# Kernel optimization log

Measured on AMD Instinct MI355X. Metric: run time of the kernel, lower is better.

Reference implementation:

```python
import jax, jax.numpy as jnp
import numpy as np

N_POINTS = 1_000_000
NUM_PILLARS = 30_000
BN_EPS = 1e-3


def _bn(x, gamma, beta, mean, var):
    # eval-mode BatchNorm1d with eps=0.001
    return (x - mean) * (gamma * jax.lax.rsqrt(var + BN_EPS)) + beta


def setup_inputs() -> dict:
    key = jax.random.key(0)
    ks = jax.random.split(key, 5)
    C1, C2 = 32, 64
    return {
        "points": jax.random.normal(ks[0], (N_POINTS, 5), dtype=jnp.float32),
        "f_center": jax.random.normal(ks[1], (N_POINTS, 3), dtype=jnp.float32),
        "unq_inv": jax.random.randint(ks[2], (N_POINTS,), 0, NUM_PILLARS, dtype=jnp.int32),
        "W1": jax.random.normal(ks[3], (7, C1), dtype=jnp.float32) * 0.1,
        "g1": jnp.ones((C1,), jnp.float32),
        "b1": jnp.zeros((C1,), jnp.float32),
        "m1": jnp.zeros((C1,), jnp.float32),
        "v1": jnp.ones((C1,), jnp.float32),
        "W2": jax.random.normal(ks[4], (C2, C1), dtype=jnp.float32) * 0.1,
        "g2": jnp.ones((C1,), jnp.float32),
        "b2": jnp.zeros((C1,), jnp.float32),
        "m2": jnp.zeros((C1,), jnp.float32),
        "v2": jnp.ones((C1,), jnp.float32),
    }


def reference(points, f_center, unq_inv, W1, g1, b1, m1, v1, W2, g2, b2, m2, v2):
    # gen_feat: concat(f_center, points[:,1:]) -> Linear(no bias) -> BN -> ReLU
    feats = jnp.concatenate([f_center, points[:, 1:]], axis=-1)  # [N, 7]
    h = jnp.maximum(_bn(feats @ W1, g1, b1, m1, v1), 0.0)        # [N, 32]

    # scatter_mean over pillars, then gather back and concat
    seg_sum = jax.ops.segment_sum(h, unq_inv, num_segments=NUM_PILLARS)
    counts = jax.ops.segment_sum(jnp.ones((h.shape[0],), h.dtype), unq_inv,
                                 num_segments=NUM_PILLARS)
    seg_mean = seg_sum / jnp.maximum(counts, 1.0)[:, None]       # [P, 32]
    h2 = jnp.concatenate([h, seg_mean[unq_inv]], axis=1)         # [N, 64]

    # AVFEO: Linear(64,32,no bias) -> BN -> ReLU
    out_fc = jnp.maximum(_bn(h2 @ W2, g2, b2, m2, v2), 0.0)      # [N, 32]

    # scatter_max over pillars (empty pillars -> 0, as torch_scatter)
    seg_max = jax.ops.segment_max(out_fc, unq_inv, num_segments=NUM_PILLARS)
    return jnp.where(jnp.isfinite(seg_max), seg_max, 0.0)        # [P, 32]
```

## Files before the change

### kernel.cpp

```cpp
#include <hip/hip_runtime.h>

typedef __attribute__((ext_vector_type(8))) short short8;
typedef __attribute__((ext_vector_type(4))) float floatx4;

static constexpr float EPS = 1e-3f;

#define CAP8  88
#define NB1   64
#define CCAP  20480
#define FCAP  384

#define P_W1F  0
#define P_B1F  224
#define P_W2L  256
#define P_B2F  1280
#define P_W2UT 1312
#define PREP_F 2048

__device__ __forceinline__ unsigned short f2bf(float x) {
  unsigned u = __float_as_uint(x);
  u += 0x7FFFu + ((u >> 16) & 1u);
  return (unsigned short)(u >> 16);
}

__global__ __launch_bounds__(256)
void k_prep_row8(const float* __restrict__ points, const float* __restrict__ fc,
                 int* __restrict__ tails, float* __restrict__ row8,
                 const float* __restrict__ W1, const float* __restrict__ g1,
                 const float* __restrict__ b1, const float* __restrict__ m1,
                 const float* __restrict__ v1,
                 const float* __restrict__ W2, const float* __restrict__ g2,
                 const float* __restrict__ b2, const float* __restrict__ m2,
                 const float* __restrict__ v2, float* __restrict__ prep,
                 int N) {
  const int gid = blockIdx.x * 256 + threadIdx.x;
  if (gid < 4096) tails[gid] = 0;
  if (blockIdx.x == 0) {
    const int t = threadIdx.x;
    for (int i = t; i < 224; i += 256) {
      int c = i & 31;
      prep[P_W1F + i] = W1[i] * (g1[c] * rsqrtf(v1[c] + EPS));
    }
    if (t < 32) {
      float s1 = g1[t] * rsqrtf(v1[t] + EPS);
      float s2 = g2[t] * rsqrtf(v2[t] + EPS);
      prep[P_B1F + t] = b1[t] - m1[t] * s1;
      prep[P_B2F + t] = b2[t] - m2[t] * s2;
    }
    unsigned short* wt = (unsigned short*)(prep + P_W2UT);
    for (int i = t; i < 1024; i += 256) {
      int k = i >> 5, c = i & 31;
      float s2 = g2[c] * rsqrtf(v2[c] + EPS);
      prep[P_W2L + i] = W2[(32 + k) * 32 + c] * s2;
      wt[c * 32 + k] = f2bf(W2[k * 32 + c] * s2);
    }
  }
  if (gid < N) {
    const size_t i = (size_t)gid;
    float4 a, b;
    a.x = fc[3 * i];     a.y = fc[3 * i + 1]; a.z = fc[3 * i + 2];
    a.w = points[5 * i + 1];
    b.x = points[5 * i + 2]; b.y = points[5 * i + 3]; b.z = points[5 * i + 4];
    b.w = 0.f;
    float4* dst = (float4*)(row8 + i * 8);
    dst[0] = a;
    dst[1] = b;
  }
}

__global__ __launch_bounds__(256)
void k_bin1(const int* __restrict__ unq, int* __restrict__ tails,
            int2* __restrict__ cbuf, int N) {
  __shared__ int2 orec[2048];
  __shared__ int dst[2048];
  __shared__ int hist[NB1], sbase[NB1], gbase[NB1];

  const int t = threadIdx.x;
  const int tile0 = blockIdx.x * 2048;
  const int ntile = min(2048, N - tile0);
  if (t < NB1) hist[t] = 0;
  __syncthreads();

  int pv[8], rr[8], bb[8];
  const int lbase = t * 8;
  if (lbase < ntile) {
    const int4* u4 = (const int4*)(unq + tile0 + lbase);
    int4 ua = u4[0], ub = u4[1];
    pv[0] = ua.x; pv[1] = ua.y; pv[2] = ua.z; pv[3] = ua.w;
    pv[4] = ub.x; pv[5] = ub.y; pv[6] = ub.z; pv[7] = ub.w;
#pragma unroll
    for (int u = 0; u < 8; ++u) {
      bb[u] = pv[u] >> 9;
      rr[u] = atomicAdd(&hist[bb[u]], 1);
    }
  } else {
#pragma unroll
    for (int u = 0; u < 8; ++u) bb[u] = -1;
  }
  __syncthreads();

  if (t < 64) {
    const int h = hist[t];
    int x = h;
    for (int d = 1; d < 64; d <<= 1) {
      int y = __shfl_up(x, d);
      if (t >= d) x += y;
    }
    sbase[t] = x - h;
    gbase[t] = (h > 0) ? atomicAdd(&tails[t], h) : 0;
  }
  __syncthreads();

  if (bb[0] >= 0) {
#pragma unroll
    for (int u = 0; u < 8; ++u) {
      const int s = sbase[bb[u]] + rr[u];
      orec[s] = make_int2(tile0 + lbase + u, pv[u]);
      const int gd = gbase[bb[u]] + rr[u];
      dst[s] = (gd < CCAP) ? (bb[u] * CCAP + gd) : -1;
    }
  }
  __syncthreads();

  for (int k = t; k < ntile; k += 256) {
    const int d = dst[k];
    if (d >= 0) cbuf[d] = orec[k];
  }
}

__global__ __launch_bounds__(256)
void k_bin2(const int* __restrict__ tails_ro, int* __restrict__ tails,
            const int2* __restrict__ cbuf, int2* __restrict__ fgbuf) {
  __shared__ int2 orec[2048];
  __shared__ int dst[2048];
  __shared__ int hist[64], sbase[64], gbase[64];

  const int b = blockIdx.x / 10, tl = blockIdx.x % 10;
  const int n_b = min(tails_ro[b], CCAP);
  const int tile0 = tl * 2048;
  const int ntile = min(2048, n_b - tile0);
  if (ntile <= 0) return;

  const int t = threadIdx.x;
  if (t < 64) hist[t] = 0;
  __syncthreads();

  const int2* src = cbuf + (size_t)b * CCAP + tile0;
  int2 rv[8];
  int rr[8], bb[8];
  const int lbase = t * 8;
#pragma unroll
  for (int u = 0; u < 8; ++u) {
    const int j = lbase + u;
    if (j < ntile) {
      rv[u] = src[j];
      bb[u] = (rv[u].y >> 3) & 63;
      rr[u] = atomicAdd(&hist[bb[u]], 1);
    } else bb[u] = -1;
  }
  __syncthreads();

  if (t < 64) {
    const int h = hist[t];
    int x = h;
    for (int d = 1; d < 64; d <<= 1) {
      int y = __shfl_up(x, d);
      if (t >= d) x += y;
    }
    sbase[t] = x - h;
    gbase[t] = (h > 0) ? atomicAdd(&tails[64 + (b << 6) + t], h) : 0;
  }
  __syncthreads();

#pragma unroll
  for (int u = 0; u < 8; ++u) {
    if (bb[u] >= 0) {
      const int s = sbase[bb[u]] + rr[u];
      orec[s] = rv[u];
      const int gd = gbase[bb[u]] + rr[u];
      dst[s] = (gd < FCAP) ? (((b << 6) + bb[u]) * FCAP + gd) : -1;
    }
  }
  __syncthreads();

  for (int k = t; k < ntile; k += 256) {
    const int d = dst[k];
    if (d >= 0) fgbuf[d] = orec[k];
  }
}

__global__ __launch_bounds__(512)
void k_pillar(const float* __restrict__ prep, const int* __restrict__ tails,
              const int2* __restrict__ fgbuf, const float* __restrict__ row8,
              float* __restrict__ out, int npil) {
  __shared__ __align__(16) float rec[FCAP][8];
  __shared__ unsigned short ord[8][CAP8];
  __shared__ __align__(16) unsigned short hbuf[8 * CAP8 * 32];
  __shared__ __align__(16) unsigned short w2t[1024];
  __shared__ __align__(16) float sumb[8][32];
  __shared__ int cnt8[8];

  const int t = threadIdx.x;
  if (t < 256) ((uint2*)w2t)[t] = ((const uint2*)(prep + P_W2UT))[t];
  if (t < 8) cnt8[t] = 0;
  __syncthreads();

  const int fb = blockIdx.x;
  const int nrec = min(tails[64 + fb], FCAP);

  const int2* src = fgbuf + (size_t)fb * FCAP;
  for (int j = t; j < nrec; j += 512) {
    const int2 r = src[j];
    const floatx4* rp = (const floatx4*)(row8 + (size_t)r.x * 8);
    ((floatx4*)rec[j])[0] = rp[0];
    ((floatx4*)rec[j])[1] = rp[1];
    const int pl = r.y & 7;
    const int slot = atomicAdd(&cnt8[pl], 1);
    if (slot < CAP8) ord[pl][slot] = (unsigned short)j;
  }
  __syncthreads();

  const int w = t >> 6, lane = t & 63;
  const int c = lane & 31, half = lane >> 5;
  const int p = fb * 8 + w;
  if (p >= npil) return;
  int n = cnt8[w];
  n = n < CAP8 ? n : CAP8;

  float w1c[7];
#pragma unroll
  for (int r = 0; r < 7; ++r) w1c[r] = prep[P_W1F + r * 32 + c];
  const float b1c = prep[P_B1F + c];
  const float b2c = prep[P_B2F + c];

  float ps = 0.f;
  const int rbase = w * CAP8;
#pragma unroll 2
  for (int s = half; s < n; s += 2) {
    const int j = ord[w][s];
    const floatx4 fa = *(const floatx4*)rec[j];
    const floatx4 fv = *(const floatx4*)(rec[j] + 4);
    float d = fa.x * w1c[0];
    d = fmaf(fa.y, w1c[1], d);
    d = fmaf(fa.z, w1c[2], d);
    d = fmaf(fa.w, w1c[3], d);
    d = fmaf(fv.x, w1c[4], d);
    d = fmaf(fv.y, w1c[5], d);
    d = fmaf(fv.z, w1c[6], d);
    const float h = fmaxf(d + b1c, 0.f);
    ps += h;
    const int row = rbase + s;
    hbuf[row * 32 + (c ^ (((row >> 1) & 3) << 3))] = f2bf(h);
  }
  ps += __shfl_xor(ps, 32);
  if (half == 0) sumb[w][c] = ps;
  __builtin_amdgcn_wave_barrier();

  float acc = 0.f;
  const floatx4* sb4 = (const floatx4*)sumb[w];
#pragma unroll
  for (int kq = 0; kq < 8; ++kq) {
    floatx4 sv = sb4[kq];
    acc = fmaf(sv.x, prep[P_W2L + (kq * 4 + 0) * 32 + c], acc);
    acc = fmaf(sv.y, prep[P_W2L + (kq * 4 + 1) * 32 + c], acc);
    acc = fmaf(sv.z, prep[P_W2L + (kq * 4 + 2) * 32 + c], acc);
    acc = fmaf(sv.w, prep[P_W2L + (kq * 4 + 3) * 32 + c], acc);
  }
  const float inv_n = (n > 0) ? 1.f / (float)n : 1.f;
  const float pc = fmaf(inv_n, acc, b2c);

  const int m16 = lane & 15, q4 = lane >> 4;
  const short8 bf0 = *(const short8*)(w2t + m16 * 32 + q4 * 8);
  const short8 bf1 = *(const short8*)(w2t + (m16 + 16) * 32 + q4 * 8);
  float m0 = -INFINITY, m1 = -INFINITY;
  const int ntiles = (n + 15) >> 4;
  for (int rt = 0; rt < ntiles; ++rt) {
    const int row = rbase + rt * 16 + m16;
    short8 af = *(const short8*)(hbuf + row * 32 +
                                 ((q4 ^ ((row >> 1) & 3)) << 3));
    floatx4 z = {0.f, 0.f, 0.f, 0.f};
    floatx4 a0 = __builtin_amdgcn_mfma_f32_16x16x32_bf16(af, bf0, z, 0, 0, 0);
    floatx4 a1 = __builtin_amdgcn_mfma_f32_16x16x32_bf16(af, bf1, z, 0, 0, 0);
    const int rowb = rt * 16 + q4 * 4;
#pragma unroll
    for (int r = 0; r < 4; ++r) {
      if (rowb + r < n) {
        m0 = fmaxf(m0, a0[r]);
        m1 = fmaxf(m1, a1[r]);
      }
    }
  }
  m0 = fmaxf(m0, __shfl_xor(m0, 16));
  m0 = fmaxf(m0, __shfl_xor(m0, 32));
  m1 = fmaxf(m1, __shfl_xor(m1, 16));
  m1 = fmaxf(m1, __shfl_xor(m1, 32));

  if (lane < 32) {
    float q = (lane & 16) ? m1 : m0;
    out[p * 32 + lane] = fmaxf(q + pc, 0.f);
  }
}

extern "C" void kernel_launch(void* const* d_in, const int* in_sizes, int n_in,
                              void* d_out, int out_size, void* d_ws, size_t ws_size,
                              hipStream_t stream) {
  const float* points = (const float*)d_in[0];
  const float* fc     = (const float*)d_in[1];
  const int*   unq    = (const int*)d_in[2];
  const float* W1 = (const float*)d_in[3];
  const float* g1 = (const float*)d_in[4];
  const float* b1 = (const float*)d_in[5];
  const float* m1 = (const float*)d_in[6];
  const float* v1 = (const float*)d_in[7];
  const float* W2 = (const float*)d_in[8];
  const float* g2 = (const float*)d_in[9];
  const float* b2 = (const float*)d_in[10];
  const float* m2 = (const float*)d_in[11];
  const float* v2 = (const float*)d_in[12];

  const int N    = in_sizes[0] / 5;
  const int NPIL = out_size / 32;

  float* ws = (float*)d_ws;
  int* tails = (int*)ws;
  float* prep = ws + 4096;
  float* row8 = prep + PREP_F;
  int2* cbuf = (int2*)(row8 + (size_t)N * 8);
  int2* fgbuf = cbuf + (size_t)59 * CCAP;

  k_prep_row8<<<(N + 255) / 256, 256, 0, stream>>>(points, fc, tails, row8,
                                                   W1, g1, b1, m1, v1,
                                                   W2, g2, b2, m2, v2, prep, N);

  k_bin1<<<(N + 2047) / 2048, 256, 0, stream>>>(unq, tails, cbuf, N);

  k_bin2<<<59 * 10, 256, 0, stream>>>(tails, tails, cbuf, fgbuf);

  const int nfb = (NPIL + 7) / 8;
  k_pillar<<<nfb, 512, 0, stream>>>(prep, tails, fgbuf, row8,
                                    (float*)d_out, NPIL);
}
```

Measured before the change: 167.9 us.

## Carry packed fp16 point features through binning passes instead of indirect row gather

Removes the separate row8 staging pass. k_bin1 now reads points and f_center directly, packs the seven features as fp16 with the pillar id in the top 16 bits, and moves 16-byte records through both binning passes. k_pillar then reads features straight from its bucket instead of gathering rows by point index. This avoids one full pass over the points and the random gathers, at the cost of wider scattered records, fp16 precision on inputs, and a pillar id limited to 16 bits. CAP8 is also lowered, which shrinks LDS use.

```diff
diff --git a/kernel.cpp b/kernel.cpp
--- a/kernel.cpp
+++ b/kernel.cpp
@@ -1,11 +1,12 @@
 #include <hip/hip_runtime.h>
 
 typedef __attribute__((ext_vector_type(8))) short short8;
+typedef __attribute__((ext_vector_type(8))) _Float16 f16x8;
 typedef __attribute__((ext_vector_type(4))) float floatx4;
 
 static constexpr float EPS = 1e-3f;
 
-#define CAP8  88
+#define CAP8  80
 #define NB1   64
 #define CCAP  20480
 #define FCAP  384
@@ -22,19 +23,22 @@
   u += 0x7FFFu + ((u >> 16) & 1u);
   return (unsigned short)(u >> 16);
 }
+__device__ __forceinline__ unsigned pkh(float a, float b) {
+  unsigned short ha = __builtin_bit_cast(unsigned short, (_Float16)a);
+  unsigned short hb = __builtin_bit_cast(unsigned short, (_Float16)b);
+  return (unsigned)ha | ((unsigned)hb << 16);
+}
 
 __global__ __launch_bounds__(256)
-void k_prep_row8(const float* __restrict__ points, const float* __restrict__ fc,
-                 int* __restrict__ tails, float* __restrict__ row8,
+void k_zero_prep(int* __restrict__ tails,
                  const float* __restrict__ W1, const float* __restrict__ g1,
                  const float* __restrict__ b1, const float* __restrict__ m1,
                  const float* __restrict__ v1,
                  const float* __restrict__ W2, const float* __restrict__ g2,
                  const float* __restrict__ b2, const float* __restrict__ m2,
-                 const float* __restrict__ v2, float* __restrict__ prep,
-                 int N) {
-  const int gid = blockIdx.x * 256 + threadIdx.x;
-  if (gid < 4096) tails[gid] = 0;
+                 const float* __restrict__ v2, float* __restrict__ prep) {
+  const int id = blockIdx.x * 256 + threadIdx.x;
+  if (id < 4096) tails[id] = 0;
   if (blockIdx.x == 0) {
     const int t = threadIdx.x;
     for (int i = t; i < 224; i += 256) {
@@ -55,23 +59,13 @@
       wt[c * 32 + k] = f2bf(W2[k * 32 + c] * s2);
     }
   }
-  if (gid < N) {
-    const size_t i = (size_t)gid;
-    float4 a, b;
-    a.x = fc[3 * i];     a.y = fc[3 * i + 1]; a.z = fc[3 * i + 2];
-    a.w = points[5 * i + 1];
-    b.x = points[5 * i + 2]; b.y = points[5 * i + 3]; b.z = points[5 * i + 4];
-    b.w = 0.f;
-    float4* dst = (float4*)(row8 + i * 8);
-    dst[0] = a;
-    dst[1] = b;
-  }
 }
 
 __global__ __launch_bounds__(256)
-void k_bin1(const int* __restrict__ unq, int* __restrict__ tails,
-            int2* __restrict__ cbuf, int N) {
-  __shared__ int2 orec[2048];
+void k_bin1(const float* __restrict__ points, const float* __restrict__ fc,
+            const int* __restrict__ unq, int* __restrict__ tails,
+            uint4* __restrict__ cbuf, int N) {
+  __shared__ uint4 orec[2048];
   __shared__ int dst[2048];
   __shared__ int hist[NB1], sbase[NB1], gbase[NB1];
 
@@ -81,15 +75,27 @@
   if (t < NB1) hist[t] = 0;
   __syncthreads();
 
-  int pv[8], rr[8], bb[8];
+  uint4 rv[8];
+  int rr[8], bb[8];
   const int lbase = t * 8;
   if (lbase < ntile) {
-    const int4* u4 = (const int4*)(unq + tile0 + lbase);
-    int4 ua = u4[0], ub = u4[1];
-    pv[0] = ua.x; pv[1] = ua.y; pv[2] = ua.z; pv[3] = ua.w;
-    pv[4] = ub.x; pv[5] = ub.y; pv[6] = ub.z; pv[7] = ub.w;
+    const int i0 = tile0 + lbase;
+    float f3v[24], p5v[40];
+    const float4* fca = (const float4*)(fc + (size_t)i0 * 3);
+#pragma unroll
+    for (int u = 0; u < 6; ++u) ((float4*)f3v)[u] = fca[u];
+    const float4* pta = (const float4*)(points + (size_t)i0 * 5);
+#pragma unroll
+    for (int u = 0; u < 10; ++u) ((float4*)p5v)[u] = pta[u];
+    const int4* u4 = (const int4*)(unq + i0);
+    const int4 ua = u4[0], ub = u4[1];
+    const int pv[8] = {ua.x, ua.y, ua.z, ua.w, ub.x, ub.y, ub.z, ub.w};
 #pragma unroll
     for (int u = 0; u < 8; ++u) {
+      rv[u].x = pkh(f3v[3 * u], f3v[3 * u + 1]);
+      rv[u].y = pkh(f3v[3 * u + 2], p5v[5 * u + 1]);
+      rv[u].z = pkh(p5v[5 * u + 2], p5v[5 * u + 3]);
+      rv[u].w = (pkh(p5v[5 * u + 4], 0.f) & 0xFFFFu) | ((unsigned)pv[u] << 16);
       bb[u] = pv[u] >> 9;
       rr[u] = atomicAdd(&hist[bb[u]], 1);
     }
@@ -115,7 +121,7 @@
 #pragma unroll
     for (int u = 0; u < 8; ++u) {
       const int s = sbase[bb[u]] + rr[u];
-      orec[s] = make_int2(tile0 + lbase + u, pv[u]);
+      orec[s] = rv[u];
       const int gd = gbase[bb[u]] + rr[u];
       dst[s] = (gd < CCAP) ? (bb[u] * CCAP + gd) : -1;
     }
@@ -130,8 +136,8 @@
 
 __global__ __launch_bounds__(256)
 void k_bin2(const int* __restrict__ tails_ro, int* __restrict__ tails,
-            const int2* __restrict__ cbuf, int2* __restrict__ fgbuf) {
-  __shared__ int2 orec[2048];
+            const uint4* __restrict__ cbuf, uint4* __restrict__ fgbuf) {
+  __shared__ uint4 orec[2048];
   __shared__ int dst[2048];
   __shared__ int hist[64], sbase[64], gbase[64];
 
@@ -145,8 +151,8 @@
   if (t < 64) hist[t] = 0;
   __syncthreads();
 
-  const int2* src = cbuf + (size_t)b * CCAP + tile0;
-  int2 rv[8];
+  const uint4* src = cbuf + (size_t)b * CCAP + tile0;
+  uint4 rv[8];
   int rr[8], bb[8];
   const int lbase = t * 8;
 #pragma unroll
@@ -154,7 +160,8 @@
     const int j = lbase + u;
     if (j < ntile) {
       rv[u] = src[j];
-      bb[u] = (rv[u].y >> 3) & 63;
+      const int p = (int)(rv[u].w >> 16);
+      bb[u] = (p >> 3) & 63;
       rr[u] = atomicAdd(&hist[bb[u]], 1);
     } else bb[u] = -1;
   }
@@ -191,9 +198,9 @@
 
 __global__ __launch_bounds__(512)
 void k_pillar(const float* __restrict__ prep, const int* __restrict__ tails,
-              const int2* __restrict__ fgbuf, const float* __restrict__ row8,
-              float* __restrict__ out, int npil) {
-  __shared__ __align__(16) float rec[FCAP][8];
+              const uint4* __restrict__ fgbuf, float* __restrict__ out,
+              int npil) {
+  __shared__ __align__(16) uint4 rec[FCAP];
   __shared__ unsigned short ord[8][CAP8];
   __shared__ __align__(16) unsigned short hbuf[8 * CAP8 * 32];
   __shared__ __align__(16) unsigned short w2t[1024];
@@ -208,13 +215,11 @@
   const int fb = blockIdx.x;
   const int nrec = min(tails[64 + fb], FCAP);
 
-  const int2* src = fgbuf + (size_t)fb * FCAP;
+  const uint4* src = fgbuf + (size_t)fb * FCAP;
   for (int j = t; j < nrec; j += 512) {
-    const int2 r = src[j];
-    const floatx4* rp = (const floatx4*)(row8 + (size_t)r.x * 8);
-    ((floatx4*)rec[j])[0] = rp[0];
-    ((floatx4*)rec[j])[1] = rp[1];
-    const int pl = r.y & 7;
+    const uint4 r = src[j];
+    rec[j] = r;
+    const int pl = (int)(r.w >> 16) & 7;
     const int slot = atomicAdd(&cnt8[pl], 1);
     if (slot < CAP8) ord[pl][slot] = (unsigned short)j;
   }
@@ -238,15 +243,14 @@
 #pragma unroll 2
   for (int s = half; s < n; s += 2) {
     const int j = ord[w][s];
-    const floatx4 fa = *(const floatx4*)rec[j];
-    const floatx4 fv = *(const floatx4*)(rec[j] + 4);
-    float d = fa.x * w1c[0];
-    d = fmaf(fa.y, w1c[1], d);
-    d = fmaf(fa.z, w1c[2], d);
-    d = fmaf(fa.w, w1c[3], d);
-    d = fmaf(fv.x, w1c[4], d);
-    d = fmaf(fv.y, w1c[5], d);
-    d = fmaf(fv.z, w1c[6], d);
+    const f16x8 v = *(const f16x8*)&rec[j];
+    float d = (float)v[0] * w1c[0];
+    d = fmaf((float)v[1], w1c[1], d);
+    d = fmaf((float)v[2], w1c[2], d);
+    d = fmaf((float)v[3], w1c[3], d);
+    d = fmaf((float)v[4], w1c[4], d);
+    d = fmaf((float)v[5], w1c[5], d);
+    d = fmaf((float)v[6], w1c[6], d);
     const float h = fmaxf(d + b1c, 0.f);
     ps += h;
     const int row = rbase + s;
@@ -324,19 +328,16 @@
   float* ws = (float*)d_ws;
   int* tails = (int*)ws;
   float* prep = ws + 4096;
-  float* row8 = prep + PREP_F;
-  int2* cbuf = (int2*)(row8 + (size_t)N * 8);
-  int2* fgbuf = cbuf + (size_t)59 * CCAP;
-
-  k_prep_row8<<<(N + 255) / 256, 256, 0, stream>>>(points, fc, tails, row8,
-                                                   W1, g1, b1, m1, v1,
-                                                   W2, g2, b2, m2, v2, prep, N);
-
-  k_bin1<<<(N + 2047) / 2048, 256, 0, stream>>>(unq, tails, cbuf, N);
+  uint4* cbuf = (uint4*)(prep + PREP_F);
+  uint4* fgbuf = cbuf + (size_t)59 * CCAP;
+
+  k_zero_prep<<<16, 256, 0, stream>>>(tails, W1, g1, b1, m1, v1,
+                                      W2, g2, b2, m2, v2, prep);
+
+  k_bin1<<<(N + 2047) / 2048, 256, 0, stream>>>(points, fc, unq, tails, cbuf, N);
 
   k_bin2<<<59 * 10, 256, 0, stream>>>(tails, tails, cbuf, fgbuf);
 
   const int nfb = (NPIL + 7) / 8;
-  k_pillar<<<nfb, 512, 0, stream>>>(prep, tails, fgbuf, row8,
-                                    (float*)d_out, NPIL);
-}
+  k_pillar<<<nfb, 512, 0, stream>>>(prep, tails, fgbuf, (float*)d_out, NPIL);
+}
```

Result: slower. 182.6 us (+8.8%).

## Compute first pillar linear layer with fp16 MFMA instead of scalar FMAs

Applied to the files above, without the earlier changes.

The first Linear+BN+ReLU in the pillar kernel moves from per-lane scalar FMA loops to 16x16x32 fp16 MFMA instructions. Point records are now packed into shared memory as fp16 with a constant-1 column that carries the folded bias. The prep kernel builds a transposed fp16 W1 matrix with the bias folded in, and CAP8 is reduced to 80 so the extra shared buffer fits. Inputs and first-layer weights drop from fp32 to fp16, which costs precision, and pillars with more than 80 points are truncated earlier than before.

```diff
diff --git a/kernel.cpp b/kernel.cpp
--- a/kernel.cpp
+++ b/kernel.cpp
@@ -1,11 +1,12 @@
 #include <hip/hip_runtime.h>
 
 typedef __attribute__((ext_vector_type(8))) short short8;
+typedef __attribute__((ext_vector_type(8))) _Float16 f16x8;
 typedef __attribute__((ext_vector_type(4))) float floatx4;
 
 static constexpr float EPS = 1e-3f;
 
-#define CAP8  88
+#define CAP8  80
 #define NB1   64
 #define CCAP  20480
 #define FCAP  384
@@ -15,12 +16,18 @@
 #define P_W2L  256
 #define P_B2F  1280
 #define P_W2UT 1312
-#define PREP_F 2048
+#define P_W1H  1824
+#define PREP_F 2560
 
 __device__ __forceinline__ unsigned short f2bf(float x) {
   unsigned u = __float_as_uint(x);
   u += 0x7FFFu + ((u >> 16) & 1u);
   return (unsigned short)(u >> 16);
+}
+__device__ __forceinline__ unsigned pkh(float a, float b) {
+  unsigned short ha = __builtin_bit_cast(unsigned short, (_Float16)a);
+  unsigned short hb = __builtin_bit_cast(unsigned short, (_Float16)b);
+  return (unsigned)ha | ((unsigned)hb << 16);
 }
 
 __global__ __launch_bounds__(256)
@@ -48,11 +55,16 @@
       prep[P_B2F + t] = b2[t] - m2[t] * s2;
     }
     unsigned short* wt = (unsigned short*)(prep + P_W2UT);
+    unsigned short* w1h = (unsigned short*)(prep + P_W1H);
     for (int i = t; i < 1024; i += 256) {
       int k = i >> 5, c = i & 31;
       float s2 = g2[c] * rsqrtf(v2[c] + EPS);
       prep[P_W2L + i] = W2[(32 + k) * 32 + c] * s2;
       wt[c * 32 + k] = f2bf(W2[k * 32 + c] * s2);
+      float s1c = g1[c] * rsqrtf(v1[c] + EPS);
+      float wv = (k < 7) ? W1[k * 32 + c] * s1c
+               : (k == 7) ? (b1[c] - m1[c] * s1c) : 0.f;
+      w1h[c * 32 + k] = __builtin_bit_cast(unsigned short, (_Float16)wv);
     }
   }
   if (gid < N) {
@@ -193,15 +205,18 @@
 void k_pillar(const float* __restrict__ prep, const int* __restrict__ tails,
               const int2* __restrict__ fgbuf, const float* __restrict__ row8,
               float* __restrict__ out, int npil) {
-  __shared__ __align__(16) float rec[FCAP][8];
-  __shared__ unsigned short ord[8][CAP8];
+  __shared__ __align__(16) uint4 rec[FCAP];
+  __shared__ __align__(16) unsigned short ord[8][CAP8];
   __shared__ __align__(16) unsigned short hbuf[8 * CAP8 * 32];
   __shared__ __align__(16) unsigned short w2t[1024];
+  __shared__ __align__(16) unsigned short w1t[1024];
   __shared__ __align__(16) float sumb[8][32];
   __shared__ int cnt8[8];
 
   const int t = threadIdx.x;
   if (t < 256) ((uint2*)w2t)[t] = ((const uint2*)(prep + P_W2UT))[t];
+  if (t < 256) ((uint2*)w1t)[t] = ((const uint2*)(prep + P_W1H))[t];
+  if (t < 320) ((unsigned*)ord)[t] = 0;
   if (t < 8) cnt8[t] = 0;
   __syncthreads();
 
@@ -212,8 +227,13 @@
   for (int j = t; j < nrec; j += 512) {
     const int2 r = src[j];
     const floatx4* rp = (const floatx4*)(row8 + (size_t)r.x * 8);
-    ((floatx4*)rec[j])[0] = rp[0];
-    ((floatx4*)rec[j])[1] = rp[1];
+    const floatx4 a = rp[0], b = rp[1];
+    uint4 rv;
+    rv.x = pkh(a.x, a.y);
+    rv.y = pkh(a.z, a.w);
+    rv.z = pkh(b.x, b.y);
+    rv.w = pkh(b.z, 1.0f);
+    rec[j] = rv;
     const int pl = r.y & 7;
     const int slot = atomicAdd(&cnt8[pl], 1);
     if (slot < CAP8) ord[pl][slot] = (unsigned short)j;
@@ -221,39 +241,51 @@
   __syncthreads();
 
   const int w = t >> 6, lane = t & 63;
-  const int c = lane & 31, half = lane >> 5;
+  const int c = lane & 31;
+  const int m16 = lane & 15, q4 = lane >> 4;
   const int p = fb * 8 + w;
   if (p >= npil) return;
   int n = cnt8[w];
   n = n < CAP8 ? n : CAP8;
 
-  float w1c[7];
-#pragma unroll
-  for (int r = 0; r < 7; ++r) w1c[r] = prep[P_W1F + r * 32 + c];
-  const float b1c = prep[P_B1F + c];
+  const f16x8 wb0 = *(const f16x8*)(w1t + m16 * 32 + q4 * 8);
+  const f16x8 wb1 = *(const f16x8*)(w1t + (m16 + 16) * 32 + q4 * 8);
+  const short8 bf0 = *(const short8*)(w2t + m16 * 32 + q4 * 8);
+  const short8 bf1 = *(const short8*)(w2t + (m16 + 16) * 32 + q4 * 8);
   const float b2c = prep[P_B2F + c];
 
-  float ps = 0.f;
+  float sa = 0.f, sb = 0.f;
   const int rbase = w * CAP8;
-#pragma unroll 2
-  for (int s = half; s < n; s += 2) {
-    const int j = ord[w][s];
-    const floatx4 fa = *(const floatx4*)rec[j];
-    const floatx4 fv = *(const floatx4*)(rec[j] + 4);
-    float d = fa.x * w1c[0];
-    d = fmaf(fa.y, w1c[1], d);
-    d = fmaf(fa.z, w1c[2], d);
-    d = fmaf(fa.w, w1c[3], d);
-    d = fmaf(fv.x, w1c[4], d);
-    d = fmaf(fv.y, w1c[5], d);
-    d = fmaf(fv.z, w1c[6], d);
-    const float h = fmaxf(d + b1c, 0.f);
-    ps += h;
-    const int row = rbase + s;
-    hbuf[row * 32 + (c ^ (((row >> 1) & 3) << 3))] = f2bf(h);
-  }
-  ps += __shfl_xor(ps, 32);
-  if (half == 0) sumb[w][c] = ps;
+  const int ntiles = (n + 15) >> 4;
+  for (int rt = 0; rt < ntiles; ++rt) {
+    const int j = ord[w][rt * 16 + m16];
+    const f16x8 af = *(const f16x8*)&rec[j];
+    floatx4 z = {0.f, 0.f, 0.f, 0.f};
+    floatx4 d0 = __builtin_amdgcn_mfma_f32_16x16x32_f16(af, wb0, z, 0, 0, 0);
+    floatx4 d1 = __builtin_amdgcn_mfma_f32_16x16x32_f16(af, wb1, z, 0, 0, 0);
+    const int rowb = rt * 16 + q4 * 4;
+#pragma unroll
+    for (int r = 0; r < 4; ++r) {
+      if (rowb + r < n) {
+        const float h0 = fmaxf(d0[r], 0.f);
+        const float h1 = fmaxf(d1[r], 0.f);
+        sa += h0;
+        sb += h1;
+        const int row = rbase + rowb + r;
+        const int sw = ((row >> 1) & 3) << 3;
+        hbuf[row * 32 + (m16 ^ sw)] = f2bf(h0);
+        hbuf[row * 32 + ((m16 + 16) ^ sw)] = f2bf(h1);
+      }
+    }
+  }
+  sa += __shfl_xor(sa, 16);
+  sa += __shfl_xor(sa, 32);
+  sb += __shfl_xor(sb, 16);
+  sb += __shfl_xor(sb, 32);
+  if (q4 == 0) {
+    sumb[w][m16] = sa;
+    sumb[w][m16 + 16] = sb;
+  }
   __builtin_amdgcn_wave_barrier();
 
   float acc = 0.f;
@@ -269,11 +301,7 @@
   const float inv_n = (n > 0) ? 1.f / (float)n : 1.f;
   const float pc = fmaf(inv_n, acc, b2c);
 
-  const int m16 = lane & 15, q4 = lane >> 4;
-  const short8 bf0 = *(const short8*)(w2t + m16 * 32 + q4 * 8);
-  const short8 bf1 = *(const short8*)(w2t + (m16 + 16) * 32 + q4 * 8);
   float m0 = -INFINITY, m1 = -INFINITY;
-  const int ntiles = (n + 15) >> 4;
   for (int rt = 0; rt < ntiles; ++rt) {
     const int row = rbase + rt * 16 + m16;
     short8 af = *(const short8*)(hbuf + row * 32 +
```

Measured after the change: 159.3 us. 1.05x faster.
